# Performance work log

Measured on AMD Instinct MI355X. Metric: run time of the kernel, lower is better.

Reference implementation:

```python
import jax, jax.numpy as jnp
import numpy as np


def setup_inputs() -> dict:
    key = jax.random.key(0)
    ks = jax.random.split(key, 13)
    B, T, D, H, E, C, S = 256, 64, 512, 512, 256, 6624, 26
    s = 0.05
    return {
        "batch_H": jax.random.normal(ks[0], (B, T, D), jnp.float32),
        "text": jax.random.randint(ks[1], (B, S), 0, C, jnp.int64),
        "W_i2h": jax.random.normal(ks[2], (H, D), jnp.float32) * s,
        "W_h2h": jax.random.normal(ks[3], (H, H), jnp.float32) * s,
        "b_h2h": jax.random.normal(ks[4], (H,), jnp.float32) * s,
        "w_score": jax.random.normal(ks[5], (H,), jnp.float32) * s,
        "W_ih": jax.random.normal(ks[6], (4 * H, D + E), jnp.float32) * s,
        "W_hh": jax.random.normal(ks[7], (4 * H, H), jnp.float32) * s,
        "b_ih": jax.random.normal(ks[8], (4 * H,), jnp.float32) * s,
        "b_hh": jax.random.normal(ks[9], (4 * H,), jnp.float32) * s,
        "emb": jax.random.normal(ks[10], (C, E), jnp.float32) * s,
        "W_gen": jax.random.normal(ks[11], (C, H), jnp.float32) * s,
        "b_gen": jax.random.normal(ks[12], (C,), jnp.float32) * s,
        "max_label_length": 25,
    }


def reference(batch_H, text, W_i2h, W_h2h, b_h2h, w_score, W_ih, W_hh,
              b_ih, b_hh, emb, W_gen, b_gen, max_label_length):
    B, T, D = batch_H.shape
    H = W_h2h.shape[0]
    num_steps = max_label_length + 1

    # i2h(batch_H) is constant across steps -> hoist out of the recurrence
    Hproj = jnp.einsum('btd,hd->bth', batch_H, W_i2h)  # [B,T,H]
    char_embs = emb[text[:, :num_steps]]               # [B,S,E]
    xs = jnp.transpose(char_embs, (1, 0, 2))           # [S,B,E]

    def step(carry, ce):
        h, c = carry
        hp = h @ W_h2h.T + b_h2h                       # [B,H]
        e = jnp.tanh(Hproj + hp[:, None, :]) @ w_score  # [B,T]
        alpha = jax.nn.softmax(e, axis=1)
        context = jnp.einsum('bt,btd->bd', alpha, batch_H)  # [B,D]
        x = jnp.concatenate([context, ce], axis=1)     # [B,D+E]
        gates = x @ W_ih.T + b_ih + h @ W_hh.T + b_hh  # [B,4H]
        i, f, g, o = jnp.split(gates, 4, axis=1)
        c_new = jax.nn.sigmoid(f) * c + jax.nn.sigmoid(i) * jnp.tanh(g)
        h_new = jax.nn.sigmoid(o) * jnp.tanh(c_new)
        return (h_new, c_new), h_new

    h0 = jnp.zeros((B, H), batch_H.dtype)
    c0 = jnp.zeros((B, H), batch_H.dtype)
    _, hs = jax.lax.scan(step, (h0, c0), xs)           # hs: [S,B,H]
    output_hiddens = jnp.transpose(hs, (1, 0, 2))      # [B,S,H]
    probs = output_hiddens @ W_gen.T + b_gen           # [B,S,C]
    return probs
```

## Files before the change

kernel.cpp:

```cpp
#include <hip/hip_runtime.h>

typedef unsigned short u16;
typedef unsigned int   u32;
typedef __attribute__((ext_vector_type(4))) float f32x4;
typedef __attribute__((ext_vector_type(8))) u16   u16x8;
typedef __attribute__((ext_vector_type(4))) u16   u16x4;
typedef __attribute__((ext_vector_type(4))) u32   u32x4;

__device__ __forceinline__ u16 f2bf(float x) {
  u32 u = __builtin_bit_cast(u32, x);
  u = (u + 0x7fffu + ((u >> 16) & 1u)) >> 16;
  return (u16)u;
}
__device__ __forceinline__ float bf2f(u16 h) {
  return __builtin_bit_cast(float, (u32)h << 16);
}
__device__ __forceinline__ float fast_sig(float x) { return 1.f / (1.f + __expf(-x)); }
__device__ __forceinline__ float fast_tanh(float x) {
  float e = __expf(2.f * x);
  return 1.f - 2.f / (e + 1.f);
}

__device__ __forceinline__ f32x4 mfma_bf16(u16x8 a, u16x8 b, f32x4 c) {
  asm volatile("v_mfma_f32_16x16x32_bf16 %0, %1, %2, %0" : "+v"(c) : "v"(a), "v"(b));
  return c;
}

__device__ __forceinline__ void gload_lds16(const void* g, void* l) {
  __builtin_amdgcn_global_load_lds(
      (__attribute__((address_space(1))) u32*)g,
      (__attribute__((address_space(3))) u32*)l, 16, 0, 0);
}

__device__ __forceinline__ void conv4(const float* __restrict__ s, u16* __restrict__ d, int i) {
  f32x4 v = *(const f32x4*)(s + i);
  u16x4 o;
  o.x = f2bf(v.x); o.y = f2bf(v.y); o.z = f2bf(v.z); o.w = f2bf(v.w);
  *(u16x4*)(d + i) = o;
}

__global__ __launch_bounds__(256) void k_prep(
    const float* __restrict__ batch_H, const float* __restrict__ W_i2h,
    const float* __restrict__ emb, const float* __restrict__ W_ih,
    const float* __restrict__ W_h2h, const float* __restrict__ W_hh,
    const float* __restrict__ W_gen, const float* __restrict__ b_ih,
    const float* __restrict__ b_hh,
    u16* __restrict__ bHb, u16* __restrict__ Wi2hb, u16* __restrict__ embb,
    u16* __restrict__ Wctxb, u16* __restrict__ Wceb, u16* __restrict__ Whcatb,
    u16* __restrict__ Wgenb, float* __restrict__ biascat,
    u16* __restrict__ hb, float* __restrict__ cst) {
  const u32 u = blockIdx.x * 256 + threadIdx.x;
  if (u < 2097152u) { conv4(batch_H, bHb, u * 4); return; }
  if (u < 2162688u) { conv4(W_i2h, Wi2hb, (u - 2097152u) * 4); return; }
  if (u < 2586624u) { conv4(emb, embb, (u - 2162688u) * 4); return; }
  if (u < 2588672u) {
    *(u16x4*)(embb + 1695744u + (u - 2586624u) * 4) = (u16x4){0, 0, 0, 0};
    return;
  }
  if (u < 2850816u) {
    int i = (u - 2588672u) * 4;
    int r = i >> 9, c = i & 511;
    f32x4 v = *(const f32x4*)(W_ih + (size_t)r * 768 + c);
    u16x4 o;
    o.x = f2bf(v.x); o.y = f2bf(v.y); o.z = f2bf(v.z); o.w = f2bf(v.w);
    *(u16x4*)(Wctxb + i) = o;
    return;
  }
  if (u < 2981888u) {
    int i = (u - 2850816u) * 4;
    int r = i >> 8, c = i & 255;
    f32x4 v = *(const f32x4*)(W_ih + (size_t)r * 768 + 512 + c);
    u16x4 o;
    o.x = f2bf(v.x); o.y = f2bf(v.y); o.z = f2bf(v.z); o.w = f2bf(v.w);
    *(u16x4*)(Wceb + i) = o;
    return;
  }
  if (u < 3309568u) {
    int i = (u - 2981888u) * 4;
    int r = i >> 9, c = i & 511;
    const float* src = (r < 512) ? (W_h2h + (size_t)r * 512 + c)
                                 : (W_hh + (size_t)(r - 512) * 512 + c);
    f32x4 v = *(const f32x4*)src;
    u16x4 o;
    o.x = f2bf(v.x); o.y = f2bf(v.y); o.z = f2bf(v.z); o.w = f2bf(v.w);
    *(u16x4*)(Whcatb + i) = o;
    return;
  }
  if (u < 4161536u) {
    int i = (u - 3309568u) * 4;
    int r = i >> 9;
    if (r < 6624) conv4(W_gen, Wgenb, i);
    else *(u16x4*)(Wgenb + i) = (u16x4){0, 0, 0, 0};
    return;
  }
  if (u < 4162048u) {
    int j = (u - 4161536u) * 4;
    f32x4 a = *(const f32x4*)(b_ih + j), b = *(const f32x4*)(b_hh + j);
    f32x4 r = {a.x + b.x, a.y + b.y, a.z + b.z, a.w + b.w};
    *(f32x4*)(biascat + j) = r;
    return;
  }
  if (u < 4178432u) {
    *(u32x4*)((char*)hb + (size_t)(u - 4162048u) * 16) = (u32x4){0, 0, 0, 0};
    return;
  }
  if (u < 4211200u) {
    *(u32x4*)((char*)cst + (size_t)(u - 4178432u) * 16) = (u32x4){0, 0, 0, 0};
    return;
  }
}

template <int BM, int BN, int WM, int WN, int OUT_MODE>
__global__ __launch_bounds__(256) void gemm_bt(const u16* __restrict__ A, int lda,
                                               const u16* __restrict__ B, int ldb,
                                               const float* __restrict__ bias,
                                               float* __restrict__ Cf, u16* __restrict__ Cb,
                                               int ldc, int Nreal, int K) {
  static_assert((BM / WM) * (BN / WN) == 4, "4 waves");
  constexpr int FM = WM / 16, FN = WN / 16;
  constexpr int NWC = BN / WN;
  constexpr int CHA = (BM * 4) / 256, CHB = (BN * 4) / 256;
  __shared__ __align__(16) u16 sA[BM * 32];
  __shared__ __align__(16) u16 sB[BN * 32];
  const int tid = threadIdx.x;
  const int lane = tid & 63, wave = tid >> 6;
  const int wr = wave / NWC, wc = wave % NWC;
  const int l15 = lane & 15, lhi = lane >> 4;
  const int m0 = blockIdx.y * BM, n0 = blockIdx.x * BN;

  f32x4 acc[FM][FN];
#pragma unroll
  for (int i = 0; i < FM; ++i)
#pragma unroll
    for (int j = 0; j < FN; ++j) acc[i][j] = 0.f;

  for (int k0 = 0; k0 < K; k0 += 32) {
    __syncthreads();
#pragma unroll
    for (int j = 0; j < CHA; ++j) {
      int idx = j * 256 + tid;
      int row = idx >> 2, cc = idx & 3;
      int c = cc ^ ((row >> 1) & 3);
      gload_lds16(A + (size_t)(m0 + row) * lda + (k0 + c * 8), sA + idx * 8);
    }
#pragma unroll
    for (int j = 0; j < CHB; ++j) {
      int idx = j * 256 + tid;
      int row = idx >> 2, cc = idx & 3;
      int c = cc ^ ((row >> 1) & 3);
      gload_lds16(B + (size_t)(n0 + row) * ldb + (k0 + c * 8), sB + idx * 8);
    }
    __syncthreads();

    u16x8 av[FM], bv[FN];
#pragma unroll
    for (int mi = 0; mi < FM; ++mi) {
      int row = wr * WM + mi * 16 + l15;
      int ch = row * 4 + (lhi ^ ((row >> 1) & 3));
      av[mi] = *(const u16x8*)(sA + ch * 8);
    }
#pragma unroll
    for (int ni = 0; ni < FN; ++ni) {
      int row = wc * WN + ni * 16 + l15;
      int ch = row * 4 + (lhi ^ ((row >> 1) & 3));
      bv[ni] = *(const u16x8*)(sB + ch * 8);
    }
#pragma unroll
    for (int mi = 0; mi < FM; ++mi)
#pragma unroll
      for (int ni = 0; ni < FN; ++ni) acc[mi][ni] = mfma_bf16(av[mi], bv[ni], acc[mi][ni]);
  }

  asm volatile("s_nop 7\ns_nop 7\ns_nop 7");

#pragma unroll
  for (int mi = 0; mi < FM; ++mi) {
#pragma unroll
    for (int ni = 0; ni < FN; ++ni) {
      int col = n0 + wc * WN + ni * 16 + l15;
      if (col < Nreal) {
        float bvv = (OUT_MODE == 1) ? bias[col] : 0.f;
#pragma unroll
        for (int r = 0; r < 4; ++r) {
          int row = m0 + wr * WM + mi * 16 + lhi * 4 + r;
          float v = acc[mi][ni][r] + bvv;
          if (OUT_MODE == 2)
            Cb[(size_t)row * ldc + col] = f2bf(v);
          else
            Cf[(size_t)row * ldc + col] = v;
        }
      }
    }
  }
}

__global__ __launch_bounds__(256) void kA_hpgh(const u16* __restrict__ hb,
                                               const u16* __restrict__ Whcatb,
                                               const float* __restrict__ b_h2h,
                                               float* __restrict__ hpbuf,
                                               float* __restrict__ ghbuf) {
  __shared__ __align__(16) u16 sA[32 * 128];
  __shared__ __align__(16) u16 sB[128 * 128];
  const int tid = threadIdx.x;
  const int lane = tid & 63, wave = tid >> 6;
  const int wr = wave >> 1, wc = wave & 1;
  const int l15 = lane & 15, lhi = lane >> 4;
  const int b0 = ((int)blockIdx.x / 20) * 32, n0 = ((int)blockIdx.x % 20) * 128;

  f32x4 acc[4];
#pragma unroll
  for (int j = 0; j < 4; ++j) acc[j] = 0.f;

  for (int k0 = 0; k0 < 512; k0 += 128) {
    __syncthreads();
#pragma unroll
    for (int j = 0; j < 2; ++j) {
      int idx = j * 256 + tid, row = idx >> 4, cc = idx & 15, c = cc ^ (row & 15);
      gload_lds16(hb + (size_t)(b0 + row) * 512 + k0 + c * 8, sA + idx * 8);
    }
#pragma unroll
    for (int j = 0; j < 8; ++j) {
      int idx = j * 256 + tid, row = idx >> 4, cc = idx & 15, c = cc ^ (row & 15);
      gload_lds16(Whcatb + (size_t)(n0 + row) * 512 + k0 + c * 8, sB + idx * 8);
    }
    __syncthreads();
#pragma unroll
    for (int ks = 0; ks < 4; ++ks) {
      u16x8 av, bv[4];
      {
        int row = wr * 16 + l15;
        int ch = row * 16 + ((ks * 4 + lhi) ^ (row & 15));
        av = *(const u16x8*)(sA + ch * 8);
      }
#pragma unroll
      for (int ni = 0; ni < 4; ++ni) {
        int row = wc * 64 + ni * 16 + l15;
        int ch = row * 16 + ((ks * 4 + lhi) ^ (row & 15));
        bv[ni] = *(const u16x8*)(sB + ch * 8);
      }
#pragma unroll
      for (int ni = 0; ni < 4; ++ni) acc[ni] = mfma_bf16(av, bv[ni], acc[ni]);
    }
  }
  asm volatile("s_nop 7\ns_nop 7\ns_nop 7");
#pragma unroll
  for (int ni = 0; ni < 4; ++ni) {
    int col = n0 + wc * 64 + ni * 16 + l15;
    int rowg = b0 + wr * 16 + lhi * 4;
    if (col < 512) {
      float bvv = b_h2h[col];
#pragma unroll
      for (int r = 0; r < 4; ++r)
        hpbuf[(size_t)(rowg + r) * 512 + col] = acc[ni][r] + bvv;
    } else {
#pragma unroll
      for (int r = 0; r < 4; ++r)
        ghbuf[(size_t)(rowg + r) * 2048 + col - 512] = acc[ni][r];
    }
  }
}

__global__ __launch_bounds__(256) void kB_attn(const u16* __restrict__ Hproj,
                                               const float* __restrict__ hpbuf,
                                               const float* __restrict__ wsc,
                                               const u16* __restrict__ bh,
                                               u16* __restrict__ ctxb) {
  const int b = blockIdx.x, tid = threadIdx.x;
  __shared__ float hpsp[528];
  __shared__ float wssp[528];
  __shared__ float es[64];

  {
    int j0 = tid * 2;
    hpsp[j0 + (j0 >> 5)] = hpbuf[(size_t)b * 512 + j0];
    hpsp[j0 + 1 + ((j0 + 1) >> 5)] = hpbuf[(size_t)b * 512 + j0 + 1];
    int pi = j0 + (j0 >> 5);
    wssp[pi] = wsc[j0];
    wssp[pi + 1] = wsc[j0 + 1];
  }
  __syncthreads();

  const int ch16 = tid & 15;
  const int hbase = ch16 * 33;
  const int hc = ch16 * 32;
  float hpr[32], wsr[32];
#pragma unroll
  for (int j = 0; j < 32; ++j) {
    hpr[j] = hpsp[hbase + j];
    wsr[j] = wssp[hbase + j];
  }
#pragma unroll
  for (int tg = 0; tg < 4; ++tg) {
    int t = tg * 16 + (tid >> 4);
    const u16* hr = Hproj + (size_t)(b * 64 + t) * 512 + hc;
    float s = 0.f;
#pragma unroll
    for (int jo = 0; jo < 32; jo += 8) {
      u16x8 hv = *(const u16x8*)(hr + jo);
#pragma unroll
      for (int j = 0; j < 8; ++j) {
        float x = bf2f(hv[j]) + hpr[jo + j];
        s += fast_tanh(x) * wsr[jo + j];
      }
    }
#pragma unroll
    for (int off = 8; off; off >>= 1) s += __shfl_xor(s, off, 16);
    if (ch16 == 0) es[t] = s;
  }
  __syncthreads();
  if (tid < 64) {
    float v = es[tid];
    float m = v;
#pragma unroll
    for (int o = 32; o; o >>= 1) m = fmaxf(m, __shfl_xor(m, o, 64));
    float p = __expf(v - m);
    float su = p;
#pragma unroll
    for (int o = 32; o; o >>= 1) su += __shfl_xor(su, o, 64);
    es[tid] = p / su;
  }
  __syncthreads();
  const u16* base = bh + (size_t)b * 32768 + tid * 2;
  float c0 = 0.f, c1 = 0.f;
#pragma unroll 8
  for (int t = 0; t < 64; ++t) {
    u32 w = *(const u32*)(base + t * 512);
    float a = es[t];
    c0 = fmaf(a, bf2f((u16)(w & 0xffffu)), c0);
    c1 = fmaf(a, bf2f((u16)(w >> 16)), c1);
  }
  u32 pk = (u32)f2bf(c0) | ((u32)f2bf(c1) << 16);
  *(u32*)(ctxb + (size_t)b * 512 + tid * 2) = pk;
}

__global__ __launch_bounds__(256) void kC_gates_lstm(const u16* __restrict__ ctxb,
                                                     const u16* __restrict__ Wctxb,
                                                     const float* __restrict__ E2G,
                                                     const float* __restrict__ ghbuf,
                                                     const int* __restrict__ text,
                                                     float* __restrict__ cst,
                                                     u16* __restrict__ hb,
                                                     u16* __restrict__ hsb, int step) {
  __shared__ __align__(16) char smem[40960];
  u16* sA = (u16*)smem;
  u16* sB = (u16*)(smem + 8192);
  const int tid = threadIdx.x;
  const int lane = tid & 63, wave = tid >> 6;
  const int wr = wave >> 1, wc = wave & 1;
  const int l15 = lane & 15, lhi = lane >> 4;
  const int jt = blockIdx.x;
  const int b0 = blockIdx.y * 32;

  f32x4 acc[4];
#pragma unroll
  for (int j = 0; j < 4; ++j) acc[j] = 0.f;

  for (int k0 = 0; k0 < 512; k0 += 128) {
    __syncthreads();
#pragma unroll
    for (int j = 0; j < 2; ++j) {
      int idx = j * 256 + tid, row = idx >> 4, cc = idx & 15, c = cc ^ (row & 15);
      gload_lds16(ctxb + (size_t)(b0 + row) * 512 + k0 + c * 8, sA + idx * 8);
    }
#pragma unroll
    for (int j = 0; j < 8; ++j) {
      int idx = j * 256 + tid, row = idx >> 4, cc = idx & 15, c = cc ^ (row & 15);
      int grow = (row >> 5) * 512 + jt * 32 + (row & 31);
      gload_lds16(Wctxb + (size_t)grow * 512 + k0 + c * 8, sB + idx * 8);
    }
    __syncthreads();

#pragma unroll
    for (int ks = 0; ks < 4; ++ks) {
      u16x8 av, bv[4];
      {
        int row = wr * 16 + l15;
        int ch = row * 16 + ((ks * 4 + lhi) ^ (row & 15));
        av = *(const u16x8*)(sA + ch * 8);
      }
#pragma unroll
      for (int ni = 0; ni < 4; ++ni) {
        int row = wc * 64 + ni * 16 + l15;
        int ch = row * 16 + ((ks * 4 + lhi) ^ (row & 15));
        bv[ni] = *(const u16x8*)(sB + ch * 8);
      }
#pragma unroll
      for (int ni = 0; ni < 4; ++ni) acc[ni] = mfma_bf16(av, bv[ni], acc[ni]);
    }
  }

  asm volatile("s_nop 7\ns_nop 7\ns_nop 7");
  __syncthreads();
  float (*gsm)[132] = (float(*)[132])smem;
#pragma unroll
  for (int ni = 0; ni < 4; ++ni) {
    int col = wc * 64 + ni * 16 + l15;
    int row = wr * 16 + lhi * 4;
#pragma unroll
    for (int r = 0; r < 4; ++r) gsm[row + r][col] = acc[ni][r];
  }
  __syncthreads();

  {
    const int bl = tid >> 3, jl0 = (tid & 7) * 4;
    const int b = b0 + bl;
    const int jg0 = jt * 32 + jl0;
    const int ci = text[b * 26 + step];
    const float* gh = ghbuf + (size_t)b * 2048;
    const float* ge = E2G + (size_t)ci * 2048;
    float cn[4];
    u16 hbv[4];
#pragma unroll
    for (int q = 0; q < 4; ++q) {
      int jl = jl0 + q, j = jg0 + q;
      float gi = gsm[bl][jl]      + gh[j]        + ge[j];
      float gf = gsm[bl][32 + jl] + gh[512 + j]  + ge[512 + j];
      float gg = gsm[bl][64 + jl] + gh[1024 + j] + ge[1024 + j];
      float go = gsm[bl][96 + jl] + gh[1536 + j] + ge[1536 + j];
      float c = fast_sig(gf) * cst[(size_t)b * 512 + j] + fast_sig(gi) * fast_tanh(gg);
      cn[q] = c;
      hbv[q] = f2bf(fast_sig(go) * fast_tanh(c));
    }
    *(f32x4*)(cst + (size_t)b * 512 + jg0) = *(f32x4*)cn;
    *(u16x4*)(hb + (size_t)b * 512 + jg0) = *(u16x4*)hbv;
    *(u16x4*)(hsb + (size_t)(b * 26 + step) * 512 + jg0) = *(u16x4*)hbv;
  }
}

extern "C" void kernel_launch(void* const* d_in, const int* in_sizes, int n_in,
                              void* d_out, int out_size, void* d_ws, size_t ws_size,
                              hipStream_t stream) {
  const float* batch_H = (const float*)d_in[0];
  const int*   text    = (const int*)d_in[1];
  const float* W_i2h   = (const float*)d_in[2];
  const float* W_h2h   = (const float*)d_in[3];
  const float* b_h2h   = (const float*)d_in[4];
  const float* w_score = (const float*)d_in[5];
  const float* W_ih    = (const float*)d_in[6];
  const float* W_hh    = (const float*)d_in[7];
  const float* b_ih    = (const float*)d_in[8];
  const float* b_hh    = (const float*)d_in[9];
  const float* emb     = (const float*)d_in[10];
  const float* W_gen   = (const float*)d_in[11];
  const float* b_gen   = (const float*)d_in[12];
  float* out = (float*)d_out;

  u16* bHb   = (u16*)d_out;
  u16* Hproj = bHb + 8388608;

  char* w = (char*)d_ws;
  auto alloc = [&](size_t bytes) {
    char* p = w;
    w += (bytes + 255) & ~(size_t)255;
    return p;
  };
  u16*   Wi2hb   = (u16*)alloc(512ull * 512 * 2);
  u16*   Whcatb  = (u16*)alloc(2560ull * 512 * 2);
  u16*   Wctxb   = (u16*)alloc(2048ull * 512 * 2);
  u16*   Wceb    = (u16*)alloc(2048ull * 256 * 2);
  u16*   Wgenb   = (u16*)alloc(6656ull * 512 * 2);
  u16*   embb    = (u16*)alloc(6656ull * 256 * 2);
  float* biascat = (float*)alloc(2048ull * 4);
  u16*   ctxb    = (u16*)alloc(256ull * 512 * 2);
  u16*   hb      = (u16*)alloc(256ull * 512 * 2);
  float* cst     = (float*)alloc(256ull * 512 * 4);
  float* hpbuf   = (float*)alloc(256ull * 512 * 4);
  float* ghbuf   = (float*)alloc(256ull * 2048 * 4);
  u16*   hsb     = (u16*)alloc(6656ull * 512 * 2);
  float* E2G     = (float*)alloc(6656ull * 2048 * 4);

  k_prep<<<16450, 256, 0, stream>>>(batch_H, W_i2h, emb, W_ih, W_h2h, W_hh, W_gen,
                                    b_ih, b_hh, bHb, Wi2hb, embb, Wctxb, Wceb,
                                    Whcatb, Wgenb, biascat, hb, cst);

  gemm_bt<128, 128, 64, 64, 2><<<dim3(4, 128), 256, 0, stream>>>(
      bHb, 512, Wi2hb, 512, nullptr, nullptr, Hproj, 512, 512, 512);

  gemm_bt<128, 128, 64, 64, 1><<<dim3(16, 52), 256, 0, stream>>>(
      embb, 256, Wceb, 256, biascat, E2G, nullptr, 2048, 2048, 256);

  for (int s = 0; s < 26; ++s) {
    kA_hpgh<<<160, 256, 0, stream>>>(hb, Whcatb, b_h2h, hpbuf, ghbuf);
    kB_attn<<<256, 256, 0, stream>>>(Hproj, hpbuf, w_score, bHb, ctxb);
    kC_gates_lstm<<<dim3(16, 8), 256, 0, stream>>>(ctxb, Wctxb, E2G, ghbuf, text,
                                                   cst, hb, hsb, s);
  }

  gemm_bt<128, 128, 64, 64, 1><<<dim3(52, 52), 256, 0, stream>>>(
      hsb, 512, Wgenb, 512, b_gen, out, nullptr, 6624, 6624, 512);

  (void)in_sizes; (void)n_in; (void)out_size; (void)ws_size;
}
```

Before: 823.7 us.

## Fuse next-step h-projection GEMM into LSTM kernel with flag sync; widen GEMM K tile

Merges the per-step kA_hpgh launch into the gates/LSTM kernel: extra blocks spin-wait on per-batch-tile atomic flags set by LSTM blocks, then compute the next step's h projections into double-buffered hp/gh buffers. This removes one kernel launch per step and overlaps the next step's projection with the tail of the current LSTM work. The generic GEMM is also replaced with a 128x128 tile using K=128 per LDS stage with a wider swizzle, cutting the number of barriers. Spin-waiting relies on producer blocks being co-resident or scheduled first, which could deadlock or stall if the scheduling order changes.

```diff
diff --git a/kernel.cpp b/kernel.cpp
--- a/kernel.cpp
+++ b/kernel.cpp
@@ -48,7 +48,7 @@
     u16* __restrict__ bHb, u16* __restrict__ Wi2hb, u16* __restrict__ embb,
     u16* __restrict__ Wctxb, u16* __restrict__ Wceb, u16* __restrict__ Whcatb,
     u16* __restrict__ Wgenb, float* __restrict__ biascat,
-    u16* __restrict__ hb, float* __restrict__ cst) {
+    u16* __restrict__ hb, float* __restrict__ cst, int* __restrict__ flags) {
   const u32 u = blockIdx.x * 256 + threadIdx.x;
   if (u < 2097152u) { conv4(batch_H, bHb, u * 4); return; }
   if (u < 2162688u) { conv4(W_i2h, Wi2hb, (u - 2097152u) * 4); return; }
@@ -108,81 +108,80 @@
     *(u32x4*)((char*)cst + (size_t)(u - 4178432u) * 16) = (u32x4){0, 0, 0, 0};
     return;
   }
-}
-
-template <int BM, int BN, int WM, int WN, int OUT_MODE>
-__global__ __launch_bounds__(256) void gemm_bt(const u16* __restrict__ A, int lda,
-                                               const u16* __restrict__ B, int ldb,
-                                               const float* __restrict__ bias,
-                                               float* __restrict__ Cf, u16* __restrict__ Cb,
-                                               int ldc, int Nreal, int K) {
-  static_assert((BM / WM) * (BN / WN) == 4, "4 waves");
-  constexpr int FM = WM / 16, FN = WN / 16;
-  constexpr int NWC = BN / WN;
-  constexpr int CHA = (BM * 4) / 256, CHB = (BN * 4) / 256;
-  __shared__ __align__(16) u16 sA[BM * 32];
-  __shared__ __align__(16) u16 sB[BN * 32];
+  if (u < 4211252u) {
+    *(u32x4*)((char*)flags + (size_t)(u - 4211200u) * 16) = (u32x4){0, 0, 0, 0};
+    return;
+  }
+}
+
+template <int OUT_MODE>
+__global__ __launch_bounds__(256) void gemm_bt128(const u16* __restrict__ A, int lda,
+                                                  const u16* __restrict__ B, int ldb,
+                                                  const float* __restrict__ bias,
+                                                  float* __restrict__ Cf, u16* __restrict__ Cb,
+                                                  int ldc, int Nreal, int K) {
+  __shared__ __align__(16) u16 sA[128 * 128];
+  __shared__ __align__(16) u16 sB[128 * 128];
   const int tid = threadIdx.x;
   const int lane = tid & 63, wave = tid >> 6;
-  const int wr = wave / NWC, wc = wave % NWC;
+  const int wr = wave >> 1, wc = wave & 1;
   const int l15 = lane & 15, lhi = lane >> 4;
-  const int m0 = blockIdx.y * BM, n0 = blockIdx.x * BN;
-
-  f32x4 acc[FM][FN];
-#pragma unroll
-  for (int i = 0; i < FM; ++i)
-#pragma unroll
-    for (int j = 0; j < FN; ++j) acc[i][j] = 0.f;
-
-  for (int k0 = 0; k0 < K; k0 += 32) {
-    __syncthreads();
-#pragma unroll
-    for (int j = 0; j < CHA; ++j) {
-      int idx = j * 256 + tid;
-      int row = idx >> 2, cc = idx & 3;
-      int c = cc ^ ((row >> 1) & 3);
+  const int m0 = blockIdx.y * 128, n0 = blockIdx.x * 128;
+
+  f32x4 acc[4][4];
+#pragma unroll
+  for (int i = 0; i < 4; ++i)
+#pragma unroll
+    for (int j = 0; j < 4; ++j) acc[i][j] = 0.f;
+
+  for (int k0 = 0; k0 < K; k0 += 128) {
+    __syncthreads();
+#pragma unroll
+    for (int j = 0; j < 8; ++j) {
+      int idx = j * 256 + tid, row = idx >> 4, cc = idx & 15, c = cc ^ (row & 15);
       gload_lds16(A + (size_t)(m0 + row) * lda + (k0 + c * 8), sA + idx * 8);
     }
 #pragma unroll
-    for (int j = 0; j < CHB; ++j) {
-      int idx = j * 256 + tid;
-      int row = idx >> 2, cc = idx & 3;
-      int c = cc ^ ((row >> 1) & 3);
+    for (int j = 0; j < 8; ++j) {
+      int idx = j * 256 + tid, row = idx >> 4, cc = idx & 15, c = cc ^ (row & 15);
       gload_lds16(B + (size_t)(n0 + row) * ldb + (k0 + c * 8), sB + idx * 8);
     }
     __syncthreads();
 
-    u16x8 av[FM], bv[FN];
-#pragma unroll
-    for (int mi = 0; mi < FM; ++mi) {
-      int row = wr * WM + mi * 16 + l15;
-      int ch = row * 4 + (lhi ^ ((row >> 1) & 3));
-      av[mi] = *(const u16x8*)(sA + ch * 8);
-    }
-#pragma unroll
-    for (int ni = 0; ni < FN; ++ni) {
-      int row = wc * WN + ni * 16 + l15;
-      int ch = row * 4 + (lhi ^ ((row >> 1) & 3));
-      bv[ni] = *(const u16x8*)(sB + ch * 8);
-    }
-#pragma unroll
-    for (int mi = 0; mi < FM; ++mi)
-#pragma unroll
-      for (int ni = 0; ni < FN; ++ni) acc[mi][ni] = mfma_bf16(av[mi], bv[ni], acc[mi][ni]);
+#pragma unroll
+    for (int ks = 0; ks < 4; ++ks) {
+      u16x8 av[4], bv[4];
+#pragma unroll
+      for (int mi = 0; mi < 4; ++mi) {
+        int row = wr * 64 + mi * 16 + l15;
+        int ch = row * 16 + ((ks * 4 + lhi) ^ (row & 15));
+        av[mi] = *(const u16x8*)(sA + ch * 8);
+      }
+#pragma unroll
+      for (int ni = 0; ni < 4; ++ni) {
+        int row = wc * 64 + ni * 16 + l15;
+        int ch = row * 16 + ((ks * 4 + lhi) ^ (row & 15));
+        bv[ni] = *(const u16x8*)(sB + ch * 8);
+      }
+#pragma unroll
+      for (int mi = 0; mi < 4; ++mi)
+#pragma unroll
+        for (int ni = 0; ni < 4; ++ni) acc[mi][ni] = mfma_bf16(av[mi], bv[ni], acc[mi][ni]);
+    }
   }
 
   asm volatile("s_nop 7\ns_nop 7\ns_nop 7");
 
 #pragma unroll
-  for (int mi = 0; mi < FM; ++mi) {
-#pragma unroll
-    for (int ni = 0; ni < FN; ++ni) {
-      int col = n0 + wc * WN + ni * 16 + l15;
+  for (int mi = 0; mi < 4; ++mi) {
+#pragma unroll
+    for (int ni = 0; ni < 4; ++ni) {
+      int col = n0 + wc * 64 + ni * 16 + l15;
       if (col < Nreal) {
         float bvv = (OUT_MODE == 1) ? bias[col] : 0.f;
 #pragma unroll
         for (int r = 0; r < 4; ++r) {
-          int row = m0 + wr * WM + mi * 16 + lhi * 4 + r;
+          int row = m0 + wr * 64 + mi * 16 + lhi * 4 + r;
           float v = acc[mi][ni][r] + bvv;
           if (OUT_MODE == 2)
             Cb[(size_t)row * ldc + col] = f2bf(v);
@@ -194,18 +193,17 @@
   }
 }
 
-__global__ __launch_bounds__(256) void kA_hpgh(const u16* __restrict__ hb,
-                                               const u16* __restrict__ Whcatb,
-                                               const float* __restrict__ b_h2h,
-                                               float* __restrict__ hpbuf,
-                                               float* __restrict__ ghbuf) {
-  __shared__ __align__(16) u16 sA[32 * 128];
-  __shared__ __align__(16) u16 sB[128 * 128];
+__device__ __forceinline__ void kA_body(int b0, int n0, const u16* __restrict__ hb,
+                                        const u16* __restrict__ Whcatb,
+                                        const float* __restrict__ b_h2h,
+                                        float* __restrict__ hp, float* __restrict__ gh,
+                                        char* smem) {
+  u16* sA = (u16*)smem;
+  u16* sB = (u16*)(smem + 8192);
   const int tid = threadIdx.x;
   const int lane = tid & 63, wave = tid >> 6;
   const int wr = wave >> 1, wc = wave & 1;
   const int l15 = lane & 15, lhi = lane >> 4;
-  const int b0 = ((int)blockIdx.x / 20) * 32, n0 = ((int)blockIdx.x % 20) * 128;
 
   f32x4 acc[4];
 #pragma unroll
@@ -251,13 +249,23 @@
       float bvv = b_h2h[col];
 #pragma unroll
       for (int r = 0; r < 4; ++r)
-        hpbuf[(size_t)(rowg + r) * 512 + col] = acc[ni][r] + bvv;
+        hp[(size_t)(rowg + r) * 512 + col] = acc[ni][r] + bvv;
     } else {
 #pragma unroll
       for (int r = 0; r < 4; ++r)
-        ghbuf[(size_t)(rowg + r) * 2048 + col - 512] = acc[ni][r];
-    }
-  }
+        gh[(size_t)(rowg + r) * 2048 + col - 512] = acc[ni][r];
+    }
+  }
+}
+
+__global__ __launch_bounds__(256) void kA_hpgh(const u16* __restrict__ hb,
+                                               const u16* __restrict__ Whcatb,
+                                               const float* __restrict__ b_h2h,
+                                               float* __restrict__ hpbuf,
+                                               float* __restrict__ ghbuf) {
+  __shared__ __align__(16) char smem[40960];
+  const int b0 = ((int)blockIdx.x / 20) * 32, n0 = ((int)blockIdx.x % 20) * 128;
+  kA_body(b0, n0, hb, Whcatb, b_h2h, hpbuf, ghbuf, smem);
 }
 
 __global__ __launch_bounds__(256) void kB_attn(const u16* __restrict__ Hproj,
@@ -333,23 +341,39 @@
   *(u32*)(ctxb + (size_t)b * 512 + tid * 2) = pk;
 }
 
-__global__ __launch_bounds__(256) void kC_gates_lstm(const u16* __restrict__ ctxb,
-                                                     const u16* __restrict__ Wctxb,
-                                                     const float* __restrict__ E2G,
-                                                     const float* __restrict__ ghbuf,
-                                                     const int* __restrict__ text,
-                                                     float* __restrict__ cst,
-                                                     u16* __restrict__ hb,
-                                                     u16* __restrict__ hsb, int step) {
+__global__ __launch_bounds__(256, 2) void kCA(
+    const u16* __restrict__ ctxb, const u16* __restrict__ Wctxb,
+    const float* __restrict__ E2G, const float* __restrict__ ghbuf_cur,
+    const int* __restrict__ text, float* __restrict__ cst,
+    u16* __restrict__ hb, u16* __restrict__ hsb,
+    const u16* __restrict__ Whcatb, const float* __restrict__ b_h2h,
+    float* __restrict__ hpbuf_nxt, float* __restrict__ ghbuf_nxt,
+    int* __restrict__ flags, int step) {
   __shared__ __align__(16) char smem[40960];
+  const int tid = threadIdx.x;
+  const int bid = blockIdx.x;
+
+  if (bid >= 128) {
+    if (step == 25) return;
+    const int r = bid - 128;
+    const int b0 = (r / 20) * 32, n0 = (r % 20) * 128;
+    if (tid == 0) {
+      while (__hip_atomic_load(&flags[step * 8 + (b0 >> 5)], __ATOMIC_ACQUIRE,
+                               __HIP_MEMORY_SCOPE_AGENT) < 16)
+        __builtin_amdgcn_s_sleep(8);
+    }
+    __syncthreads();
+    kA_body(b0, n0, hb, Whcatb, b_h2h, hpbuf_nxt, ghbuf_nxt, smem);
+    return;
+  }
+
   u16* sA = (u16*)smem;
   u16* sB = (u16*)(smem + 8192);
-  const int tid = threadIdx.x;
   const int lane = tid & 63, wave = tid >> 6;
   const int wr = wave >> 1, wc = wave & 1;
   const int l15 = lane & 15, lhi = lane >> 4;
-  const int jt = blockIdx.x;
-  const int b0 = blockIdx.y * 32;
+  const int jt = bid & 15;
+  const int b0 = (bid >> 4) * 32;
 
   f32x4 acc[4];
 #pragma unroll
@@ -406,7 +430,7 @@
     const int b = b0 + bl;
     const int jg0 = jt * 32 + jl0;
     const int ci = text[b * 26 + step];
-    const float* gh = ghbuf + (size_t)b * 2048;
+    const float* gh = ghbuf_cur + (size_t)b * 2048;
     const float* ge = E2G + (size_t)ci * 2048;
     float cn[4];
     u16 hbv[4];
@@ -424,6 +448,12 @@
     *(f32x4*)(cst + (size_t)b * 512 + jg0) = *(f32x4*)cn;
     *(u16x4*)(hb + (size_t)b * 512 + jg0) = *(u16x4*)hbv;
     *(u16x4*)(hsb + (size_t)(b * 26 + step) * 512 + jg0) = *(u16x4*)hbv;
+  }
+  __syncthreads();
+  if (tid == 0) {
+    __threadfence();
+    __hip_atomic_fetch_add(&flags[step * 8 + (b0 >> 5)], 1, __ATOMIC_RELEASE,
+                           __HIP_MEMORY_SCOPE_AGENT);
   }
 }
 
@@ -464,29 +494,36 @@
   u16*   ctxb    = (u16*)alloc(256ull * 512 * 2);
   u16*   hb      = (u16*)alloc(256ull * 512 * 2);
   float* cst     = (float*)alloc(256ull * 512 * 4);
-  float* hpbuf   = (float*)alloc(256ull * 512 * 4);
-  float* ghbuf   = (float*)alloc(256ull * 2048 * 4);
+  float* hpbuf0  = (float*)alloc(256ull * 512 * 4);
+  float* hpbuf1  = (float*)alloc(256ull * 512 * 4);
+  float* ghbuf0  = (float*)alloc(256ull * 2048 * 4);
+  float* ghbuf1  = (float*)alloc(256ull * 2048 * 4);
   u16*   hsb     = (u16*)alloc(6656ull * 512 * 2);
   float* E2G     = (float*)alloc(6656ull * 2048 * 4);
-
-  k_prep<<<16450, 256, 0, stream>>>(batch_H, W_i2h, emb, W_ih, W_h2h, W_hh, W_gen,
+  int*   flags   = (int*)alloc(26ull * 8 * 4);
+
+  float* hpb[2] = {hpbuf0, hpbuf1};
+  float* ghb[2] = {ghbuf0, ghbuf1};
+
+  k_prep<<<16451, 256, 0, stream>>>(batch_H, W_i2h, emb, W_ih, W_h2h, W_hh, W_gen,
                                     b_ih, b_hh, bHb, Wi2hb, embb, Wctxb, Wceb,
-                                    Whcatb, Wgenb, biascat, hb, cst);
-
-  gemm_bt<128, 128, 64, 64, 2><<<dim3(4, 128), 256, 0, stream>>>(
+                                    Whcatb, Wgenb, biascat, hb, cst, flags);
+
+  gemm_bt128<2><<<dim3(4, 128), 256, 0, stream>>>(
       bHb, 512, Wi2hb, 512, nullptr, nullptr, Hproj, 512, 512, 512);
 
-  gemm_bt<128, 128, 64, 64, 1><<<dim3(16, 52), 256, 0, stream>>>(
+  gemm_bt128<1><<<dim3(16, 52), 256, 0, stream>>>(
       embb, 256, Wceb, 256, biascat, E2G, nullptr, 2048, 2048, 256);
 
+  kA_hpgh<<<160, 256, 0, stream>>>(hb, Whcatb, b_h2h, hpb[0], ghb[0]);
   for (int s = 0; s < 26; ++s) {
-    kA_hpgh<<<160, 256, 0, stream>>>(hb, Whcatb, b_h2h, hpbuf, ghbuf);
-    kB_attn<<<256, 256, 0, stream>>>(Hproj, hpbuf, w_score, bHb, ctxb);
-    kC_gates_lstm<<<dim3(16, 8), 256, 0, stream>>>(ctxb, Wctxb, E2G, ghbuf, text,
-                                                   cst, hb, hsb, s);
-  }
-
-  gemm_bt<128, 128, 64, 64, 1><<<dim3(52, 52), 256, 0, stream>>>(
+    kB_attn<<<256, 256, 0, stream>>>(Hproj, hpb[s & 1], w_score, bHb, ctxb);
+    kCA<<<288, 256, 0, stream>>>(ctxb, Wctxb, E2G, ghb[s & 1], text, cst, hb, hsb,
+                                 Whcatb, b_h2h, hpb[(s + 1) & 1], ghb[(s + 1) & 1],
+                                 flags, s);
+  }
+
+  gemm_bt128<1><<<dim3(52, 52), 256, 0, stream>>>(
       hsb, 512, Wgenb, 512, b_gen, out, nullptr, 6624, 6624, 512);
 
   (void)in_sizes; (void)n_in; (void)out_size; (void)ws_size;
```

After: 1.462 ms. +77.5%, slower.
